# Optimization experiments

Hardware: AMD Instinct MI355X
Metric: run time of the kernel (lower is better)

The kernel has to match this reference:

```python
import jax, jax.numpy as jnp
import numpy as np

HEADS = 8
DIM_HEAD = 32
IH = IW = 32
EPS = 1e-5


def _relative_index(ih, iw):
    # faithful reproduction of the torch buffer computation
    coords = np.stack(np.meshgrid(np.arange(ih), np.arange(iw), indexing='ij')).reshape(2, -1)  # (2, n)
    rel = coords[:, :, None] - coords[:, None, :]  # (2, n, n)
    rel[0] += ih - 1
    rel[1] += iw - 1
    rel[0] *= 2 * iw - 1
    return rel.transpose(1, 2, 0).sum(-1).reshape(-1).astype(np.int32)  # (n*n,)


def setup_inputs() -> dict:
    key = jax.random.key(0)
    ks = jax.random.split(key, 8)
    C, HID = 256, 1024
    s = 0.02
    inp = {
        'x': jax.random.normal(ks[0], (16, C, IH, IW), jnp.float32),
        'qkv_w': jax.random.normal(ks[1], (C, 3 * HEADS * DIM_HEAD), jnp.float32) * s,
        'proj_w': jax.random.normal(ks[2], (HEADS * DIM_HEAD, C), jnp.float32) * s,
        'proj_b': jnp.zeros((C,), jnp.float32),
        'ffn_w1': jax.random.normal(ks[3], (C, HID), jnp.float32) * s,
        'ffn_b1': jnp.zeros((HID,), jnp.float32),
        'ffn_w2': jax.random.normal(ks[4], (HID, C), jnp.float32) * s,
        'ffn_b2': jnp.zeros((C,), jnp.float32),
        'norm1_w': jnp.ones((C,), jnp.float32),
        'norm1_b': jnp.zeros((C,), jnp.float32),
        'norm2_w': jnp.ones((C,), jnp.float32),
        'norm2_b': jnp.zeros((C,), jnp.float32),
        'bias_table': jax.random.normal(ks[5], ((2 * IH - 1) * (2 * IW - 1), HEADS), jnp.float32) * s,
        'rel_index': jnp.asarray(_relative_index(IH, IW)),
    }
    return inp


def _layernorm(x, w, b):
    mu = jnp.mean(x, -1, keepdims=True)
    var = jnp.mean(jnp.square(x - mu), -1, keepdims=True)
    return (x - mu) * jax.lax.rsqrt(var + EPS) * w + b


def reference(x, qkv_w, proj_w, proj_b, ffn_w1, ffn_b1, ffn_w2, ffn_b2,
              norm1_w, norm1_b, norm2_w, norm2_b, bias_table, rel_index):
    B, C, H, W = x.shape
    n = H * W
    scale = DIM_HEAD ** -0.5

    # b c h w -> b n c
    xt = x.reshape(B, C, n).transpose(0, 2, 1)
    x1 = _layernorm(xt, norm1_w, norm1_b)

    qkv = x1 @ qkv_w  # (B, n, 3*inner)
    q, k, v = jnp.split(qkv, 3, axis=-1)
    def heads(t):
        return t.reshape(B, n, HEADS, DIM_HEAD).transpose(0, 2, 1, 3)  # b h n d
    q, k, v = heads(q), heads(k), heads(v)

    dots = jnp.einsum('bhid,bhjd->bhij', q, k) * scale
    # gathered relative position bias: (n*n, heads) -> (1, heads, n, n)
    bias = bias_table[rel_index].reshape(n, n, HEADS).transpose(2, 0, 1)[None]
    attn = jax.nn.softmax(dots + bias, axis=-1)
    out = jnp.einsum('bhij,bhjd->bhid', attn, v)  # b h n d
    out = out.transpose(0, 2, 1, 3).reshape(B, n, HEADS * DIM_HEAD)
    out = out @ proj_w + proj_b  # (B, n, C)

    # back to b c h w and first residual
    x1 = out.transpose(0, 2, 1).reshape(B, C, H, W)
    x3 = x1 + x

    # FFN branch
    x4 = x3.reshape(B, C, n).transpose(0, 2, 1)
    x4 = _layernorm(x4, norm2_w, norm2_b)
    x4 = jax.nn.gelu(x4 @ ffn_w1 + ffn_b1, approximate=False) @ ffn_w2 + ffn_b2
    x4 = x4.transpose(0, 2, 1).reshape(B, C, H, W)
    return x3 + x4
```

## Files before the change

kernel.cpp:

```cpp
#include <hip/hip_runtime.h>
#include <math.h>

#define BATCH 16
#define CH    256
#define NT    1024
#define NH    8
#define DH    32
#define HID   1024
#define MROWS (BATCH * NT)
#define LN_EPS 1e-5f

typedef unsigned short u16;
typedef unsigned int u32;
typedef __attribute__((ext_vector_type(8))) short short8;
typedef __attribute__((ext_vector_type(4))) float f32x4;

struct __align__(8) US4 { u16 x, y, z, w; };
struct __align__(16) F4 { float x, y, z, w; };

#define MFMA(a, b, c) __builtin_amdgcn_mfma_f32_16x16x32_bf16((a), (b), (c), 0, 0, 0)

#define LOG2E 1.4426950408889634f
#define QSCALE (0.17677669529663687f * 1.4426950408889634f)

__device__ __forceinline__ float bf2f(u16 u) {
  union { unsigned int i; float f; } v; v.i = ((unsigned int)u) << 16; return v.f;
}
__device__ __forceinline__ u16 f2bf(float f) {
  union { float f; unsigned int i; } v; v.f = f;
  unsigned int i = v.i;
  return (u16)((i + 0x7fffu + ((i >> 16) & 1u)) >> 16);
}
__device__ __forceinline__ u32 pack_bf16_pair(float lo, float hi) {
  union { float f; u32 i; } a, b; a.f = lo; b.f = hi;
#if __has_builtin(__builtin_amdgcn_perm)
  return __builtin_amdgcn_perm(b.i, a.i, 0x07060302u);
#else
  return (b.i & 0xFFFF0000u) | (a.i >> 16);
#endif
}
__device__ __forceinline__ float fast_exp2(float x) {
#if __has_builtin(__builtin_amdgcn_exp2f)
  return __builtin_amdgcn_exp2f(x);
#else
  return exp2f(x);
#endif
}
__device__ __forceinline__ void llds16(const u16* g, u16* l) {
  __builtin_amdgcn_global_load_lds(
      (const __attribute__((address_space(1))) u32*)g,
      (__attribute__((address_space(3))) u32*)l, 16, 0, 0);
}

__global__ __launch_bounds__(256) void k_transpose(const float* __restrict__ in,
                                                   u16* __restrict__ out,
                                                   int K, int N) {
  __shared__ u16 tl[64][66];
  const int t = threadIdx.x;
  const int kb = blockIdx.x * 64, nb = blockIdx.y * 64;
#pragma unroll
  for (int it = 0; it < 16; ++it) {
    int n_l = t & 63, k_l = it * 4 + (t >> 6);
    tl[k_l][n_l] = f2bf(in[(size_t)(kb + k_l) * N + nb + n_l]);
  }
  __syncthreads();
#pragma unroll
  for (int it = 0; it < 16; ++it) {
    int k_l = t & 63, n_l = it * 4 + (t >> 6);
    out[(size_t)(nb + n_l) * K + kb + k_l] = tl[k_l][n_l];
  }
}

__global__ __launch_bounds__(256) void k_prep_bias(const float* __restrict__ table,
                                                   const int* __restrict__ rel,
                                                   u16* __restrict__ biasB) {
  __shared__ u16 tl[64][66];
  const int t = threadIdx.x;
  const int jb = (blockIdx.x & 15) * 64, ib = (blockIdx.x >> 4) * 64;
  int idxs[16];
#pragma unroll
  for (int it = 0; it < 16; ++it) {
    int j_l = t & 63, i_l = it * 4 + (t >> 6);
    idxs[it] = rel[(size_t)(ib + i_l) * NT + jb + j_l];
  }
  u32* outd = (u32*)biasB;
  for (int h = 0; h < NH; ++h) {
    __syncthreads();
#pragma unroll
    for (int it = 0; it < 16; ++it) {
      int j_l = t & 63, i_l = it * 4 + (t >> 6);
      tl[j_l][i_l] = f2bf(table[(size_t)idxs[it] * NH + h] * LOG2E);
    }
    __syncthreads();
#pragma unroll
    for (int it = 0; it < 8; ++it) {
      int i_l = t & 63, jp_l = it * 4 + (t >> 6);
      u32 v = (u32)tl[2 * jp_l][i_l] | ((u32)tl[2 * jp_l + 1][i_l] << 16);
      outd[(size_t)h * 524288 + (size_t)((jb >> 1) + jp_l) * 1024 + ib + i_l] = v;
    }
  }
}

__global__ __launch_bounds__(256) void k_ln1(const float* __restrict__ x,
                                             const float* __restrict__ w,
                                             const float* __restrict__ b,
                                             u16* __restrict__ x1) {
  __shared__ u16 tile[CH][68];
  __shared__ float red_s[4][64], red_q[4][64], mu_s[64], rs_s[64];
  const int t = threadIdx.x;
  const int bb = blockIdx.x >> 4, pb = blockIdx.x & 15;
  const int pos0 = pb * 64;
#pragma unroll
  for (int it = 0; it < 16; ++it) {
    int c = it * 16 + (t >> 4), p4 = (t & 15) * 4;
    F4 v = *(const F4*)(x + ((size_t)bb * CH + c) * NT + pos0 + p4);
    US4 o; o.x = f2bf(v.x); o.y = f2bf(v.y); o.z = f2bf(v.z); o.w = f2bf(v.w);
    *(US4*)&tile[c][p4] = o;
  }
  __syncthreads();
  {
    int pos = t & 63, g = t >> 6;
    float s = 0.f, q = 0.f;
#pragma unroll 8
    for (int cc = 0; cc < 64; ++cc) {
      float v = bf2f(tile[g * 64 + cc][pos]);
      s += v; q += v * v;
    }
    red_s[g][pos] = s; red_q[g][pos] = q;
  }
  __syncthreads();
  if (t < 64) {
    float s = red_s[0][t] + red_s[1][t] + red_s[2][t] + red_s[3][t];
    float q = red_q[0][t] + red_q[1][t] + red_q[2][t] + red_q[3][t];
    float mu = s * (1.f / CH);
    float var = q * (1.f / CH) - mu * mu;
    mu_s[t] = mu;
    rs_s[t] = rsqrtf(fmaxf(var, 0.f) + LN_EPS);
  }
  __syncthreads();
  {
    const int c = t;
    const float wv = w[c], bv = b[c];
    for (int pos = 0; pos < 64; ++pos) {
      float v = (bf2f(tile[c][pos]) - mu_s[pos]) * rs_s[pos] * wv + bv;
      x1[((size_t)bb * NT + pos0 + pos) * CH + c] = f2bf(v);
    }
  }
}

template <int K>
__device__ __forceinline__ void gemm128(const u16* __restrict__ A,
                                        const u16* __restrict__ Bt,
                                        int r0, int c0, int tid,
                                        u16* lA, u16* lB,
                                        f32x4 acc[4][4]) {
  const int wave = tid >> 6, lane = tid & 63;
  const int wm = (wave >> 1) * 64, wn = (wave & 1) * 64;
  const int l16 = lane & 15, quad = lane >> 4;
  const int srow = lane >> 2;
  const int scol = (lane & 3) * 8;
  const u16* gA0 = A + (size_t)(r0 + wave * 16 + srow) * K + scol;
  const u16* gA1 = A + (size_t)(r0 + wave * 16 + 64 + srow) * K + scol;
  const u16* gB0 = Bt + (size_t)(c0 + wave * 16 + srow) * K + scol;
  const u16* gB1 = Bt + (size_t)(c0 + wave * 16 + 64 + srow) * K + scol;
  u16* lA0 = lA + (wave * 16) * 32;
  u16* lA1 = lA + (wave * 16 + 64) * 32;
  u16* lB0 = lB + (wave * 16) * 32;
  u16* lB1 = lB + (wave * 16 + 64) * 32;
  for (int k0 = 0; k0 < K; k0 += 32) {
    __syncthreads();
    llds16(gA0 + k0, lA0);
    llds16(gA1 + k0, lA1);
    llds16(gB0 + k0, lB0);
    llds16(gB1 + k0, lB1);
    __syncthreads();
    short8 af[4], bf[4];
#pragma unroll
    for (int i = 0; i < 4; ++i)
      af[i] = *(const short8*)&lA[(wm + i * 16 + l16) * 32 + quad * 8];
#pragma unroll
    for (int j = 0; j < 4; ++j)
      bf[j] = *(const short8*)&lB[(wn + j * 16 + l16) * 32 + quad * 8];
#pragma unroll
    for (int i = 0; i < 4; ++i)
#pragma unroll
      for (int j = 0; j < 4; ++j)
        acc[i][j] = MFMA(af[i], bf[j], acc[i][j]);
  }
}

#define GEMM_PROLOGUE(KVAL, APTR, BPTR)                                  \
  __shared__ __align__(16) u16 lA[128 * 32];                             \
  __shared__ __align__(16) u16 lB[128 * 32];                             \
  const int tid = threadIdx.x;                                           \
  const int wave = tid >> 6, lane = tid & 63;                            \
  const int wm = (wave >> 1) * 64, wn = (wave & 1) * 64;                 \
  const int l16 = lane & 15, quad = lane >> 4;                           \
  const int r0 = blockIdx.x * 128, c0 = blockIdx.y * 128;                \
  f32x4 acc[4][4];                                                       \
  _Pragma("unroll") for (int i = 0; i < 4; ++i)                          \
  _Pragma("unroll") for (int j = 0; j < 4; ++j) acc[i][j] = 0.f;         \
  gemm128<KVAL>(APTR, BPTR, r0, c0, tid, lA, lB, acc);

__global__ __launch_bounds__(256) void k_gemm_qkv(const u16* __restrict__ x1,
                                                  const u16* __restrict__ wT,
                                                  u16* __restrict__ q,
                                                  u16* __restrict__ k,
                                                  u16* __restrict__ vT) {
  GEMM_PROLOGUE(CH, x1, wT)
#pragma unroll
  for (int j = 0; j < 4; ++j) {
    int col = c0 + wn + j * 16 + l16;
    int which = col >> 8, rem = col & 255, h = rem >> 5, dd = rem & 31;
#pragma unroll
    for (int i = 0; i < 4; ++i) {
      int row0 = r0 + wm + i * 16 + quad * 4;
      int bb = row0 >> 10, pos = row0 & 1023;
      if (which == 2) {
        US4 o;
        o.x = f2bf(acc[i][j][0]); o.y = f2bf(acc[i][j][1]);
        o.z = f2bf(acc[i][j][2]); o.w = f2bf(acc[i][j][3]);
        *(US4*)(vT + (((size_t)bb * NH + h) * DH + dd) * NT + pos) = o;
      } else {
        u16* dst = (which == 0) ? q : k;
        float mul = (which == 0) ? QSCALE : 1.0f;
#pragma unroll
        for (int r = 0; r < 4; ++r)
          dst[(((size_t)bb * NH + h) * NT + pos + r) * DH + dd] =
              f2bf(acc[i][j][r] * mul);
      }
    }
  }
}

__global__ __launch_bounds__(256) void k_gemm_proj(const u16* __restrict__ ao,
                                                   const u16* __restrict__ wT,
                                                   const float* __restrict__ pb,
                                                   const float* __restrict__ x,
                                                   u16* __restrict__ x3) {
  GEMM_PROLOGUE(CH, ao, wT)
#pragma unroll
  for (int j = 0; j < 4; ++j) {
    int col = c0 + wn + j * 16 + l16;
    float bias = pb[col];
#pragma unroll
    for (int i = 0; i < 4; ++i) {
      int row0 = r0 + wm + i * 16 + quad * 4;
      int bb = row0 >> 10, pos = row0 & 1023;
#pragma unroll
      for (int r = 0; r < 4; ++r) {
        float val = acc[i][j][r] + bias + x[((size_t)bb * CH + col) * NT + pos + r];
        x3[(size_t)(row0 + r) * CH + col] = f2bf(val);
      }
    }
  }
}

__global__ __launch_bounds__(256) void k_gemm_ffn1(const u16* __restrict__ a,
                                                   const u16* __restrict__ wT,
                                                   const float* __restrict__ b1,
                                                   u16* __restrict__ hmat) {
  GEMM_PROLOGUE(CH, a, wT)
#pragma unroll
  for (int j = 0; j < 4; ++j) {
    int col = c0 + wn + j * 16 + l16;
    float bias = b1[col];
#pragma unroll
    for (int i = 0; i < 4; ++i) {
      int row0 = r0 + wm + i * 16 + quad * 4;
#pragma unroll
      for (int r = 0; r < 4; ++r) {
        float v = acc[i][j][r] + bias;
        float g = 0.5f * v * (1.0f + erff(v * 0.70710678118654752f));
        hmat[(size_t)(row0 + r) * HID + col] = f2bf(g);
      }
    }
  }
}

__global__ __launch_bounds__(256) void k_gemm_ffn2(const u16* __restrict__ a,
                                                   const u16* __restrict__ wT,
                                                   const float* __restrict__ b2,
                                                   u16* __restrict__ x4) {
  GEMM_PROLOGUE(HID, a, wT)
#pragma unroll
  for (int j = 0; j < 4; ++j) {
    int col = c0 + wn + j * 16 + l16;
    float bias = b2[col];
#pragma unroll
    for (int i = 0; i < 4; ++i) {
      int row0 = r0 + wm + i * 16 + quad * 4;
#pragma unroll
      for (int r = 0; r < 4; ++r)
        x4[(size_t)(row0 + r) * CH + col] = f2bf(acc[i][j][r] + bias);
    }
  }
}

__global__ __launch_bounds__(256) void k_attn(const u16* __restrict__ q,
                                              const u16* __restrict__ k,
                                              const u16* __restrict__ vT,
                                              const u16* __restrict__ biasB,
                                              u16* __restrict__ ao) {
  __shared__ u16 Ks[256][40];
  __shared__ u16 Vt[32][264];
  __shared__ u16 Ps[4][16][40];
  const int tid = threadIdx.x;
  const int wave = tid >> 6, lane = tid & 63;
  const int quad = lane >> 4, l16 = lane & 15;
  const int bh = blockIdx.x >> 4, qt = blockIdx.x & 15;
  const int h = bh & 7, bb = bh >> 3;
  const int i0 = qt * 64 + wave * 16;

  short8 aq = *(const short8*)(q + ((size_t)bh * NT + i0 + l16) * DH + quad * 8);
  const u16* bias_h = biasB + (size_t)h * 1048576 + (size_t)(i0 + quad * 4) * 2;

  float l_loc[4] = {0.f, 0.f, 0.f, 0.f};
  f32x4 acc0 = 0.f, acc1 = 0.f;

  for (int chunk = 0; chunk < 4; ++chunk) {
    __syncthreads();
    const int rbase = chunk * 256;
    {
      const int srow = tid >> 3, sdd = (tid & 7) * 4;
#pragma unroll
      for (int it = 0; it < 8; ++it) {
        int rl = it * 32 + srow;
        int rowL = (rl & ~31) | ((rl & 31) >> 1) | ((rl & 1) << 4);
        US4 kv = *(const US4*)(k + ((size_t)bh * NT + rbase + rl) * DH + sdd);
        *(US4*)&Ks[rowL][sdd] = kv;
      }
      const int j4 = (tid & 63) * 4;
#pragma unroll
      for (int it = 0; it < 8; ++it) {
        int d = it * 4 + wave;
        US4 vv = *(const US4*)(vT + ((size_t)bh * DH + d) * NT + rbase + j4);
        *(US4*)&Vt[d][j4] = vv;
      }
    }
    __syncthreads();

#pragma unroll 2
    for (int j0 = 0; j0 < 256; j0 += 32) {
      short8 bk0 = *(const short8*)&Ks[j0 + l16][quad * 8];
      short8 bk1 = *(const short8*)&Ks[j0 + 16 + l16][quad * 8];
      short8 be = *(const short8*)(bias_h +
                   ((size_t)((rbase + j0) >> 1) + l16) * 2048);
      const u16* bep = (const u16*)&be;
      f32x4 c0, c1;
#pragma unroll
      for (int r = 0; r < 4; ++r) {
        c0[r] = bf2f(bep[2 * r]);
        c1[r] = bf2f(bep[2 * r + 1]);
      }
      f32x4 s0 = MFMA(aq, bk0, c0);
      f32x4 s1 = MFMA(aq, bk1, c1);
      u32 packed[4];
#pragma unroll
      for (int r = 0; r < 4; ++r) {
        float p0 = fast_exp2(s0[r]);
        float p1 = fast_exp2(s1[r]);
        l_loc[r] += p0 + p1;
        packed[r] = pack_bf16_pair(p0, p1);
      }
      u32* psw = (u32*)&Ps[wave][0][0];
#pragma unroll
      for (int r = 0; r < 4; ++r) psw[(quad * 4 + r) * 20 + l16] = packed[r];
      short8 ap  = *(const short8*)&Ps[wave][l16][quad * 8];
      short8 bv0 = *(const short8*)&Vt[l16][j0 + quad * 8];
      short8 bv1 = *(const short8*)&Vt[16 + l16][j0 + quad * 8];
      acc0 = MFMA(ap, bv0, acc0);
      acc1 = MFMA(ap, bv1, acc1);
    }
  }
#pragma unroll
  for (int mask = 1; mask <= 8; mask <<= 1) {
#pragma unroll
    for (int r = 0; r < 4; ++r) l_loc[r] += __shfl_xor(l_loc[r], mask);
  }
#pragma unroll
  for (int r = 0; r < 4; ++r) {
    float inv = 1.0f / l_loc[r];
    int row = i0 + quad * 4 + r;
    u16* o = ao + ((size_t)bb * NT + row) * CH + h * DH;
    o[l16]      = f2bf(acc0[r] * inv);
    o[16 + l16] = f2bf(acc1[r] * inv);
  }
}

__global__ __launch_bounds__(256) void k_ln2(const u16* __restrict__ x3,
                                             const float* __restrict__ w,
                                             const float* __restrict__ b,
                                             u16* __restrict__ x4ln) {
  const int wave = threadIdx.x >> 6, lane = threadIdx.x & 63;
  const size_t row = (size_t)blockIdx.x * 4 + wave;
  US4 u = *(const US4*)(x3 + row * CH + lane * 4);
  float v0 = bf2f(u.x), v1 = bf2f(u.y), v2 = bf2f(u.z), v3 = bf2f(u.w);
  float s = v0 + v1 + v2 + v3;
  float qq = v0 * v0 + v1 * v1 + v2 * v2 + v3 * v3;
#pragma unroll
  for (int mask = 1; mask <= 32; mask <<= 1) {
    s += __shfl_xor(s, mask);
    qq += __shfl_xor(qq, mask);
  }
  float mu = s * (1.f / CH);
  float var = qq * (1.f / CH) - mu * mu;
  float rs = rsqrtf(fmaxf(var, 0.f) + LN_EPS);
  F4 uw = *(const F4*)(w + lane * 4);
  F4 ub = *(const F4*)(b + lane * 4);
  US4 o;
  o.x = f2bf((v0 - mu) * rs * uw.x + ub.x);
  o.y = f2bf((v1 - mu) * rs * uw.y + ub.y);
  o.z = f2bf((v2 - mu) * rs * uw.z + ub.z);
  o.w = f2bf((v3 - mu) * rs * uw.w + ub.w);
  *(US4*)(x4ln + row * CH + lane * 4) = o;
}

__global__ __launch_bounds__(256) void k_add_t(const u16* __restrict__ x3,
                                               const u16* __restrict__ x4,
                                               float* __restrict__ out) {
  __shared__ float tl[64][66];
  const int t = threadIdx.x;
  const int bb = blockIdx.x >> 6;
  const int pb = (blockIdx.x >> 2) & 15, cb = blockIdx.x & 3;
  const int pos0 = pb * 64, c0 = cb * 64;
#pragma unroll
  for (int it = 0; it < 16; ++it) {
    int c_l = t & 63, p_l = it * 4 + (t >> 6);
    size_t ro = ((size_t)bb * NT + pos0 + p_l) * CH + c0 + c_l;
    tl[p_l][c_l] = bf2f(x3[ro]) + bf2f(x4[ro]);
  }
  __syncthreads();
#pragma unroll
  for (int it = 0; it < 16; ++it) {
    int p_l = t & 63, c_l = it * 4 + (t >> 6);
    out[((size_t)bb * CH + c0 + c_l) * NT + pos0 + p_l] = tl[p_l][c_l];
  }
}

extern "C" void kernel_launch(void* const* d_in, const int* in_sizes, int n_in,
                              void* d_out, int out_size, void* d_ws, size_t ws_size,
                              hipStream_t stream) {
  const float* x       = (const float*)d_in[0];
  const float* qkv_w   = (const float*)d_in[1];
  const float* proj_w  = (const float*)d_in[2];
  const float* proj_b  = (const float*)d_in[3];
  const float* ffn_w1  = (const float*)d_in[4];
  const float* ffn_b1  = (const float*)d_in[5];
  const float* ffn_w2  = (const float*)d_in[6];
  const float* ffn_b2  = (const float*)d_in[7];
  const float* norm1_w = (const float*)d_in[8];
  const float* norm1_b = (const float*)d_in[9];
  const float* norm2_w = (const float*)d_in[10];
  const float* norm2_b = (const float*)d_in[11];
  const float* btab    = (const float*)d_in[12];
  const int* rel       = (const int*)d_in[13];
  float* out = (float*)d_out;

  char* ws = (char*)d_ws;
  size_t off = 0;
  auto alloc = [&](size_t bytes) { char* p = ws + off; off += bytes; return p; };
  u16* qkv_wT  = (u16*)alloc((size_t)768 * 256 * 2);
  u16* proj_wT = (u16*)alloc((size_t)256 * 256 * 2);
  u16* w1T     = (u16*)alloc((size_t)1024 * 256 * 2);
  u16* w2T     = (u16*)alloc((size_t)256 * 1024 * 2);
  u16* biasB   = (u16*)alloc((size_t)NH * NT * NT * 2);
  u16* qm      = (u16*)alloc((size_t)MROWS * CH * 2);
  u16* km      = (u16*)alloc((size_t)MROWS * CH * 2);
  u16* vm      = (u16*)alloc((size_t)MROWS * CH * 2);
  u16* bufX    = (u16*)alloc((size_t)MROWS * CH * 2);
  u16* x3      = (u16*)alloc((size_t)MROWS * CH * 2);
  u16* ffn_h = biasB;
  u16* x4ln  = vm;
  u16* x1 = bufX;
  u16* ao = bufX;
  u16* x4 = bufX;
  (void)ws_size; (void)in_sizes; (void)n_in; (void)out_size;

  k_transpose<<<dim3(4, 12), 256, 0, stream>>>(qkv_w, qkv_wT, 256, 768);
  k_transpose<<<dim3(4, 4), 256, 0, stream>>>(proj_w, proj_wT, 256, 256);
  k_transpose<<<dim3(4, 16), 256, 0, stream>>>(ffn_w1, w1T, 256, 1024);
  k_transpose<<<dim3(16, 4), 256, 0, stream>>>(ffn_w2, w2T, 1024, 256);
  k_prep_bias<<<256, 256, 0, stream>>>(btab, rel, biasB);
  k_ln1<<<BATCH * 16, 256, 0, stream>>>(x, norm1_w, norm1_b, x1);
  k_gemm_qkv<<<dim3(MROWS / 128, 6), 256, 0, stream>>>(x1, qkv_wT, qm, km, vm);
  k_attn<<<BATCH * NH * 16, 256, 0, stream>>>(qm, km, vm, biasB, ao);
  k_gemm_proj<<<dim3(MROWS / 128, 2), 256, 0, stream>>>(ao, proj_wT, proj_b, x, x3);
  k_ln2<<<MROWS / 4, 256, 0, stream>>>(x3, norm2_w, norm2_b, x4ln);
  k_gemm_ffn1<<<dim3(MROWS / 128, 8), 256, 0, stream>>>(x4ln, w1T, ffn_b1, ffn_h);
  k_gemm_ffn2<<<dim3(MROWS / 128, 2), 256, 0, stream>>>(ffn_h, w2T, ffn_b2, x4);
  k_add_t<<<BATCH * 16 * 4, 256, 0, stream>>>(x3, x4, out);
}
```

Before: 271.9 us.

## Compute transposed scores in attention to keep P in registers, drop LDS roundtrip

The attention kernel now computes S^T = K·Q^T, so each lane's MFMA output already matches the A-operand layout of a 16x16x16 bf16 MFMA for the PV product. This removes the per-iteration write and read of P through shared memory. The relative-position bias buffer is re-laid out in 32-column tiles so each lane loads contiguous bias values, and the bias prep kernel is simplified accordingly. The trade-off is four narrower MFMAs instead of two for PV, extra shuffles for the row-sum, and an uncoalesced strided write pattern in the prep kernel.

```diff
diff --git a/kernel.cpp b/kernel.cpp
--- a/kernel.cpp
+++ b/kernel.cpp
@@ -13,12 +13,14 @@
 typedef unsigned short u16;
 typedef unsigned int u32;
 typedef __attribute__((ext_vector_type(8))) short short8;
+typedef __attribute__((ext_vector_type(4))) short short4v;
 typedef __attribute__((ext_vector_type(4))) float f32x4;
 
 struct __align__(8) US4 { u16 x, y, z, w; };
 struct __align__(16) F4 { float x, y, z, w; };
 
 #define MFMA(a, b, c) __builtin_amdgcn_mfma_f32_16x16x32_bf16((a), (b), (c), 0, 0, 0)
+#define MFMA16(a, b, c) __builtin_amdgcn_mfma_f32_16x16x16bf16_1k((a), (b), (c), 0, 0, 0)
 
 #define LOG2E 1.4426950408889634f
 #define QSCALE (0.17677669529663687f * 1.4426950408889634f)
@@ -33,18 +35,14 @@
 }
 __device__ __forceinline__ u32 pack_bf16_pair(float lo, float hi) {
   union { float f; u32 i; } a, b; a.f = lo; b.f = hi;
-#if __has_builtin(__builtin_amdgcn_perm)
+#if defined(__HIP_DEVICE_COMPILE__)
   return __builtin_amdgcn_perm(b.i, a.i, 0x07060302u);
 #else
   return (b.i & 0xFFFF0000u) | (a.i >> 16);
 #endif
 }
 __device__ __forceinline__ float fast_exp2(float x) {
-#if __has_builtin(__builtin_amdgcn_exp2f)
-  return __builtin_amdgcn_exp2f(x);
-#else
   return exp2f(x);
-#endif
 }
 __device__ __forceinline__ void llds16(const u16* g, u16* l) {
   __builtin_amdgcn_global_load_lds(
@@ -73,30 +71,17 @@
 
 __global__ __launch_bounds__(256) void k_prep_bias(const float* __restrict__ table,
                                                    const int* __restrict__ rel,
-                                                   u16* __restrict__ biasB) {
-  __shared__ u16 tl[64][66];
+                                                   u16* __restrict__ biasL) {
   const int t = threadIdx.x;
-  const int jb = (blockIdx.x & 15) * 64, ib = (blockIdx.x >> 4) * 64;
-  int idxs[16];
-#pragma unroll
-  for (int it = 0; it < 16; ++it) {
-    int j_l = t & 63, i_l = it * 4 + (t >> 6);
-    idxs[it] = rel[(size_t)(ib + i_l) * NT + jb + j_l];
-  }
-  u32* outd = (u32*)biasB;
-  for (int h = 0; h < NH; ++h) {
-    __syncthreads();
-#pragma unroll
-    for (int it = 0; it < 16; ++it) {
-      int j_l = t & 63, i_l = it * 4 + (t >> 6);
-      tl[j_l][i_l] = f2bf(table[(size_t)idxs[it] * NH + h] * LOG2E);
-    }
-    __syncthreads();
-#pragma unroll
-    for (int it = 0; it < 8; ++it) {
-      int i_l = t & 63, jp_l = it * 4 + (t >> 6);
-      u32 v = (u32)tl[2 * jp_l][i_l] | ((u32)tl[2 * jp_l + 1][i_l] << 16);
-      outd[(size_t)h * 524288 + (size_t)((jb >> 1) + jp_l) * 1024 + ib + i_l] = v;
+  const int jt = blockIdx.x & 31, isl = blockIdx.x >> 5;
+  const int jp = t & 31, io = t >> 5;
+  for (int ib = isl * 128; ib < isl * 128 + 128; ib += 8) {
+    int i = ib + io;
+    int idx = rel[(size_t)i * NT + jt * 32 + jp];
+#pragma unroll
+    for (int h = 0; h < NH; ++h) {
+      biasL[(((size_t)h * 32 + jt) * 1024 + i) * 32 + jp] =
+          f2bf(table[(size_t)idx * NH + h] * LOG2E);
     }
   }
 }
@@ -300,11 +285,10 @@
 __global__ __launch_bounds__(256) void k_attn(const u16* __restrict__ q,
                                               const u16* __restrict__ k,
                                               const u16* __restrict__ vT,
-                                              const u16* __restrict__ biasB,
+                                              const u16* __restrict__ biasL,
                                               u16* __restrict__ ao) {
   __shared__ u16 Ks[256][40];
   __shared__ u16 Vt[32][264];
-  __shared__ u16 Ps[4][16][40];
   const int tid = threadIdx.x;
   const int wave = tid >> 6, lane = tid & 63;
   const int quad = lane >> 4, l16 = lane & 15;
@@ -313,10 +297,11 @@
   const int i0 = qt * 64 + wave * 16;
 
   short8 aq = *(const short8*)(q + ((size_t)bh * NT + i0 + l16) * DH + quad * 8);
-  const u16* bias_h = biasB + (size_t)h * 1048576 + (size_t)(i0 + quad * 4) * 2;
-
-  float l_loc[4] = {0.f, 0.f, 0.f, 0.f};
-  f32x4 acc0 = 0.f, acc1 = 0.f;
+  const u16* bias_base =
+      biasL + (((size_t)h * 32) * 1024 + (i0 + l16)) * 32 + quad * 4;
+
+  float l_loc = 0.f;
+  f32x4 accd0 = 0.f, accd1 = 0.f;
 
   for (int chunk = 0; chunk < 4; ++chunk) {
     __syncthreads();
@@ -326,9 +311,8 @@
 #pragma unroll
       for (int it = 0; it < 8; ++it) {
         int rl = it * 32 + srow;
-        int rowL = (rl & ~31) | ((rl & 31) >> 1) | ((rl & 1) << 4);
         US4 kv = *(const US4*)(k + ((size_t)bh * NT + rbase + rl) * DH + sdd);
-        *(US4*)&Ks[rowL][sdd] = kv;
+        *(US4*)&Ks[rl][sdd] = kv;
       }
       const int j4 = (tid & 63) * 4;
 #pragma unroll
@@ -342,49 +326,49 @@
 
 #pragma unroll 2
     for (int j0 = 0; j0 < 256; j0 += 32) {
-      short8 bk0 = *(const short8*)&Ks[j0 + l16][quad * 8];
-      short8 bk1 = *(const short8*)&Ks[j0 + 16 + l16][quad * 8];
-      short8 be = *(const short8*)(bias_h +
-                   ((size_t)((rbase + j0) >> 1) + l16) * 2048);
-      const u16* bep = (const u16*)&be;
-      f32x4 c0, c1;
-#pragma unroll
-      for (int r = 0; r < 4; ++r) {
-        c0[r] = bf2f(bep[2 * r]);
-        c1[r] = bf2f(bep[2 * r + 1]);
-      }
-      f32x4 s0 = MFMA(aq, bk0, c0);
-      f32x4 s1 = MFMA(aq, bk1, c1);
-      u32 packed[4];
-#pragma unroll
-      for (int r = 0; r < 4; ++r) {
-        float p0 = fast_exp2(s0[r]);
-        float p1 = fast_exp2(s1[r]);
-        l_loc[r] += p0 + p1;
-        packed[r] = pack_bf16_pair(p0, p1);
-      }
-      u32* psw = (u32*)&Ps[wave][0][0];
-#pragma unroll
-      for (int r = 0; r < 4; ++r) psw[(quad * 4 + r) * 20 + l16] = packed[r];
-      short8 ap  = *(const short8*)&Ps[wave][l16][quad * 8];
-      short8 bv0 = *(const short8*)&Vt[l16][j0 + quad * 8];
-      short8 bv1 = *(const short8*)&Vt[16 + l16][j0 + quad * 8];
-      acc0 = MFMA(ap, bv0, acc0);
-      acc1 = MFMA(ap, bv1, acc1);
-    }
-  }
-#pragma unroll
-  for (int mask = 1; mask <= 8; mask <<= 1) {
-#pragma unroll
-    for (int r = 0; r < 4; ++r) l_loc[r] += __shfl_xor(l_loc[r], mask);
-  }
+      const int jt = (rbase + j0) >> 5;
+      const u16* bl = bias_base + (size_t)jt * 32768;
+      US4 b0 = *(const US4*)bl;
+      US4 b1 = *(const US4*)(bl + 16);
+      f32x4 cc0, cc1;
+      cc0[0] = bf2f(b0.x); cc0[1] = bf2f(b0.y);
+      cc0[2] = bf2f(b0.z); cc0[3] = bf2f(b0.w);
+      cc1[0] = bf2f(b1.x); cc1[1] = bf2f(b1.y);
+      cc1[2] = bf2f(b1.z); cc1[3] = bf2f(b1.w);
+      short8 ak0 = *(const short8*)&Ks[j0 + l16][quad * 8];
+      short8 ak1 = *(const short8*)&Ks[j0 + 16 + l16][quad * 8];
+      f32x4 s0 = MFMA(ak0, aq, cc0);
+      f32x4 s1 = MFMA(ak1, aq, cc1);
+      float p00 = fast_exp2(s0[0]), p01 = fast_exp2(s0[1]);
+      float p02 = fast_exp2(s0[2]), p03 = fast_exp2(s0[3]);
+      float p10 = fast_exp2(s1[0]), p11 = fast_exp2(s1[1]);
+      float p12 = fast_exp2(s1[2]), p13 = fast_exp2(s1[3]);
+      l_loc += ((p00 + p01) + (p02 + p03)) + ((p10 + p11) + (p12 + p13));
+      union { u32 u[2]; short4v s; } pa0, pa1;
+      pa0.u[0] = pack_bf16_pair(p00, p01);
+      pa0.u[1] = pack_bf16_pair(p02, p03);
+      pa1.u[0] = pack_bf16_pair(p10, p11);
+      pa1.u[1] = pack_bf16_pair(p12, p13);
+      short4v vb00 = *(const short4v*)&Vt[l16][j0 + quad * 4];
+      short4v vb10 = *(const short4v*)&Vt[l16][j0 + 16 + quad * 4];
+      short4v vb01 = *(const short4v*)&Vt[16 + l16][j0 + quad * 4];
+      short4v vb11 = *(const short4v*)&Vt[16 + l16][j0 + 16 + quad * 4];
+      accd0 = MFMA16(pa0.s, vb00, accd0);
+      accd1 = MFMA16(pa0.s, vb01, accd1);
+      accd0 = MFMA16(pa1.s, vb10, accd0);
+      accd1 = MFMA16(pa1.s, vb11, accd1);
+    }
+  }
+  l_loc += __shfl_xor(l_loc, 16);
+  l_loc += __shfl_xor(l_loc, 32);
 #pragma unroll
   for (int r = 0; r < 4; ++r) {
-    float inv = 1.0f / l_loc[r];
+    float lr = __shfl(l_loc, quad * 4 + r);
+    float inv = 1.0f / lr;
     int row = i0 + quad * 4 + r;
     u16* o = ao + ((size_t)bb * NT + row) * CH + h * DH;
-    o[l16]      = f2bf(acc0[r] * inv);
-    o[16 + l16] = f2bf(acc1[r] * inv);
+    o[l16]      = f2bf(accd0[r] * inv);
+    o[16 + l16] = f2bf(accd1[r] * inv);
   }
 }
 
@@ -464,13 +448,13 @@
   u16* proj_wT = (u16*)alloc((size_t)256 * 256 * 2);
   u16* w1T     = (u16*)alloc((size_t)1024 * 256 * 2);
   u16* w2T     = (u16*)alloc((size_t)256 * 1024 * 2);
-  u16* biasB   = (u16*)alloc((size_t)NH * NT * NT * 2);
+  u16* biasL   = (u16*)alloc((size_t)NH * NT * NT * 2);
   u16* qm      = (u16*)alloc((size_t)MROWS * CH * 2);
   u16* km      = (u16*)alloc((size_t)MROWS * CH * 2);
   u16* vm      = (u16*)alloc((size_t)MROWS * CH * 2);
   u16* bufX    = (u16*)alloc((size_t)MROWS * CH * 2);
   u16* x3      = (u16*)alloc((size_t)MROWS * CH * 2);
-  u16* ffn_h = biasB;
+  u16* ffn_h = biasL;
   u16* x4ln  = vm;
   u16* x1 = bufX;
   u16* ao = bufX;
@@ -481,10 +465,10 @@
   k_transpose<<<dim3(4, 4), 256, 0, stream>>>(proj_w, proj_wT, 256, 256);
   k_transpose<<<dim3(4, 16), 256, 0, stream>>>(ffn_w1, w1T, 256, 1024);
   k_transpose<<<dim3(16, 4), 256, 0, stream>>>(ffn_w2, w2T, 1024, 256);
-  k_prep_bias<<<256, 256, 0, stream>>>(btab, rel, biasB);
+  k_prep_bias<<<256, 256, 0, stream>>>(btab, rel, biasL);
   k_ln1<<<BATCH * 16, 256, 0, stream>>>(x, norm1_w, norm1_b, x1);
   k_gemm_qkv<<<dim3(MROWS / 128, 6), 256, 0, stream>>>(x1, qkv_wT, qm, km, vm);
-  k_attn<<<BATCH * NH * 16, 256, 0, stream>>>(qm, km, vm, biasB, ao);
+  k_attn<<<BATCH * NH * 16, 256, 0, stream>>>(qm, km, vm, biasL, ao);
   k_gemm_proj<<<dim3(MROWS / 128, 2), 256, 0, stream>>>(ao, proj_wT, proj_b, x, x3);
   k_ln2<<<MROWS / 4, 256, 0, stream>>>(x3, norm2_w, norm2_b, x4ln);
   k_gemm_ffn1<<<dim3(MROWS / 128, 8), 256, 0, stream>>>(x4ln, w1T, ffn_b1, ffn_h);
```

Result: faster. 266.5 us (-2.0%).
